# Kernel tuning notes

Measured on AMD Instinct MI355X. Metric: run time of the kernel, lower is better.

Reference implementation:

```python
import jax, jax.numpy as jnp
import numpy as np

MAX_DISTANCE = 10
SCALE = 0.01

def distance_bias(seq_len):
    # |i - j| clamped to MAX_DISTANCE, scaled
    idx = jnp.arange(seq_len, dtype=jnp.float32)
    d = jnp.abs(idx[None, :] - idx[:, None])
    return jnp.clip(d, 0.0, MAX_DISTANCE) * SCALE  # [S, S]

def setup_inputs() -> dict:
    key = jax.random.key(0)
    k1, k2 = jax.random.split(key)
    B, S, D_IN, D_OUT = 8, 2048, 1024, 1024
    x = jax.random.normal(k1, (B, S, D_IN), dtype=jnp.float32)
    W = jax.random.normal(k2, (D_IN, D_OUT), dtype=jnp.float32) * (1.0 / np.sqrt(D_IN))
    b = jnp.zeros((D_OUT,), dtype=jnp.float32)
    return {"x": x, "W": W, "b": b}

def reference(x, W, b):
    B, S, _ = x.shape
    f = x @ W + b                                   # [B, S, H]
    e = jnp.einsum('bsd,btd->bst', f, f)            # scores [B, S, S]
    e = e + distance_bias(S)[None, :, :]
    a = jax.nn.softmax(e, axis=-1)
    out = jnp.einsum('bst,btd->bsd', a, f)          # weighted sum [B, S, H]
    return out
```

## Files before the change

### kernel.cpp

```cpp
#include <hip/hip_runtime.h>
#include <hip/hip_bf16.h>
#include <stdint.h>

typedef __attribute__((ext_vector_type(8))) short bf16x8;
typedef __attribute__((ext_vector_type(4))) float f32x4;

static __device__ __forceinline__ unsigned short f2bf(float f) {
  union { float f; unsigned int u; } v; v.f = f;
  unsigned int u = v.u;
  u += 0x7FFFu + ((u >> 16) & 1u);
  return (unsigned short)(u >> 16);
}
static __device__ __forceinline__ float bf2f(unsigned short h) {
  union { unsigned int u; float f; } v; v.u = ((unsigned int)h) << 16; return v.f;
}

typedef __attribute__((address_space(1))) void gvoid;
typedef __attribute__((address_space(3))) void lvoid;
static __device__ __forceinline__ void gload_lds16(const void* gp, void* lp) {
  __builtin_amdgcn_global_load_lds((gvoid*)gp, (lvoid*)lp, 16, 0, 0);
}

__global__ __launch_bounds__(256) void k_convX(const float* __restrict__ X,
                                               unsigned short* __restrict__ Xb) {
  size_t i = ((size_t)blockIdx.x * 256 + threadIdx.x) * 8;
  const size_t stride = (size_t)4096 * 256 * 8;
  for (; i < (size_t)16777216; i += stride) {
    float4 v0 = *(const float4*)(X + i), v1 = *(const float4*)(X + i + 4);
    unsigned short h[8];
    h[0]=f2bf(v0.x); h[1]=f2bf(v0.y); h[2]=f2bf(v0.z); h[3]=f2bf(v0.w);
    h[4]=f2bf(v1.x); h[5]=f2bf(v1.y); h[6]=f2bf(v1.z); h[7]=f2bf(v1.w);
    *(uint4*)(Xb + i) = *(uint4*)h;
  }
}

__global__ __launch_bounds__(256) void k_convW(const float* __restrict__ W,
                                               unsigned short* __restrict__ Wt) {
  __shared__ __align__(16) unsigned short lds[64][72];
  const int tid = threadIdx.x;
  const int n0 = blockIdx.x * 64, k0 = blockIdx.y * 64;
  for (int i = 0; i < 4; ++i) {
    int c = i * 256 + tid;
    int r = c >> 4, c4 = (c & 15) * 4;
    float4 v = *(const float4*)(W + (size_t)(k0 + r) * 1024 + n0 + c4);
    unsigned short* p = &lds[r][c4];
    p[0] = f2bf(v.x); p[1] = f2bf(v.y); p[2] = f2bf(v.z); p[3] = f2bf(v.w);
  }
  __syncthreads();
  for (int i = 0; i < 2; ++i) {
    int c = i * 256 + tid;
    int n = c >> 3, k8 = (c & 7) * 8;
    unsigned short tmp[8];
    for (int j = 0; j < 8; ++j) tmp[j] = lds[k8 + j][n];
    *(uint4*)(Wt + (size_t)(n0 + n) * 1024 + k0 + k8) = *(uint4*)tmp;
  }
}

__global__ __launch_bounds__(256) void k_transF(const unsigned short* __restrict__ F,
                                                unsigned short* __restrict__ Ft) {
  __shared__ __align__(16) unsigned short lds[64][72];
  const int tid = threadIdx.x;
  const int t0 = blockIdx.x * 64, d0 = blockIdx.y * 64;
  const unsigned short* Fb = F + (size_t)blockIdx.z * 2048 * 1024;
  unsigned short* Ftb = Ft + (size_t)blockIdx.z * 1024 * 2048;
  for (int i = 0; i < 2; ++i) {
    int c = i * 256 + tid;
    int r = c >> 3, d8 = (c & 7) * 8;
    *(uint4*)(&lds[r][d8]) = *(const uint4*)(Fb + (size_t)(t0 + r) * 1024 + d0 + d8);
  }
  __syncthreads();
  for (int i = 0; i < 2; ++i) {
    int c = i * 256 + tid;
    int d = c >> 3, t8 = (c & 7) * 8;
    unsigned short tmp[8];
    for (int j = 0; j < 8; ++j) tmp[j] = lds[t8 + j][d];
    *(uint4*)(Ftb + (size_t)(d0 + d) * 2048 + t0 + t8) = *(uint4*)tmp;
  }
}


template<int NT>
__device__ __forceinline__ void gemm_core(
    const unsigned short* __restrict__ Ag, int lda, int ar0,
    const unsigned short* __restrict__ Bg, int ldb, int br0,
    unsigned short* __restrict__ As, unsigned short* __restrict__ Bs,
    f32x4 (&acc)[8][4]) {
  const int tid = threadIdx.x, lane = tid & 63, wid = tid >> 6;
  const int wr = wid >> 2, wc = wid & 3;
  const int rl = lane & 15;
  const int rslot = (((lane >> 4) ^ (lane & 3) ^ ((lane >> 2) & 3))) * 8;
  const int q = tid >> 2;
  const int sslot = (((tid & 3) ^ (q & 3) ^ ((q >> 2) & 3))) * 8;

#define STAGE_T(dstbase, src, ld, r0, kt)                                      \
  _Pragma("unroll")                                                            \
  for (int r_ = 0; r_ < 2; ++r_)                                               \
    gload_lds16((src) + (size_t)((r0) + r_ * 128 + q) * (ld) + (kt) * 32 + sslot, \
                (char*)(dstbase) + r_ * 8192 + wid * 1024);

  STAGE_T(As + 0 * 8192, Ag, lda, ar0, 0)
  STAGE_T(Bs + 0 * 8192, Bg, ldb, br0, 0)
  STAGE_T(As + 1 * 8192, Ag, lda, ar0, 1)
  STAGE_T(Bs + 1 * 8192, Bg, ldb, br0, 1)
  STAGE_T(As + 2 * 8192, Ag, lda, ar0, 2)
  STAGE_T(Bs + 2 * 8192, Bg, ldb, br0, 2)
  asm volatile("s_waitcnt vmcnt(8)" ::: "memory");
  __builtin_amdgcn_s_barrier();

  bf16x8 a[4], b[4], a2[4];
  for (int t = 0; t < NT; ++t) {
    const int sl = t & 3;
    const int ps = (t + 3 < NT) ? (t + 3) : (NT - 1);
    const int psl = (t + 3) & 3;
    const unsigned short* Ab = As + sl * 8192;
    const unsigned short* Bb = Bs + sl * 8192;
#pragma unroll
    for (int m = 0; m < 4; ++m)
      a[m] = *(const bf16x8*)(Ab + (wr * 128 + m * 16 + rl) * 32 + rslot);
#pragma unroll
    for (int n = 0; n < 4; ++n)
      b[n] = *(const bf16x8*)(Bb + (wc * 64 + n * 16 + rl) * 32 + rslot);
    STAGE_T(As + psl * 8192, Ag, lda, ar0, ps)
    __builtin_amdgcn_s_barrier();
    asm volatile("s_waitcnt lgkmcnt(0)" ::: "memory");
    __builtin_amdgcn_s_setprio(1);
#pragma unroll
    for (int m = 0; m < 4; ++m)
#pragma unroll
      for (int n = 0; n < 4; ++n)
        acc[m][n] = __builtin_amdgcn_mfma_f32_16x16x32_bf16(a[m], b[n], acc[m][n], 0, 0, 0);
    __builtin_amdgcn_s_setprio(0);
    __builtin_amdgcn_s_barrier();
#pragma unroll
    for (int m = 0; m < 4; ++m)
      a2[m] = *(const bf16x8*)(Ab + (wr * 128 + (m + 4) * 16 + rl) * 32 + rslot);
    STAGE_T(Bs + psl * 8192, Bg, ldb, br0, ps)
    __builtin_amdgcn_s_barrier();
    asm volatile("s_waitcnt lgkmcnt(0)" ::: "memory");
    __builtin_amdgcn_s_setprio(1);
#pragma unroll
    for (int m = 0; m < 4; ++m)
#pragma unroll
      for (int n = 0; n < 4; ++n)
        acc[m + 4][n] = __builtin_amdgcn_mfma_f32_16x16x32_bf16(a2[m], b[n], acc[m + 4][n], 0, 0, 0);
    __builtin_amdgcn_s_setprio(0);
    asm volatile("s_waitcnt vmcnt(8)" ::: "memory");
    __builtin_amdgcn_s_barrier();
  }
  asm volatile("s_waitcnt vmcnt(0)" ::: "memory");
#undef STAGE_T
}

__global__ __launch_bounds__(512, 2) void k_gemm1(const unsigned short* __restrict__ Xb,
                                                  const unsigned short* __restrict__ Wt,
                                                  const float* __restrict__ bias,
                                                  unsigned short* __restrict__ F) {
  __shared__ __align__(16) unsigned short As[4 * 8192];
  __shared__ __align__(16) unsigned short Bs[4 * 8192];
  const int bid = blockIdx.x;
  const int swz = (bid & 7) * 32 + (bid >> 3);
  const int m0 = (swz >> 2) * 256, n0 = (swz & 3) * 256;
  f32x4 acc[8][4] = {};
  gemm_core<32>(Xb, 1024, m0, Wt, 1024, n0, As, Bs, acc);
  const int tid = threadIdx.x, lane = tid & 63, wid = tid >> 6;
  const int wr = wid >> 2, wc = wid & 3;
  const int r4 = (lane >> 4) * 4, cl = lane & 15;
#pragma unroll
  for (int n = 0; n < 4; ++n) {
    int col = n0 + wc * 64 + n * 16 + cl;
    float bv = bias[col];
#pragma unroll
    for (int m = 0; m < 8; ++m) {
      int row = m0 + wr * 128 + m * 16 + r4;
#pragma unroll
      for (int j = 0; j < 4; ++j)
        F[(size_t)(row + j) * 1024 + col] = f2bf(acc[m][n][j] + bv);
    }
  }
}

__global__ __launch_bounds__(512, 2) void k_gemm2(const unsigned short* __restrict__ F,
                                                  unsigned short* __restrict__ E) {
  __shared__ __align__(16) unsigned short As[4 * 8192];
  __shared__ __align__(16) unsigned short Bs[4 * 8192];
  const int bid = blockIdx.x;
  const int swz = (bid & 7) * 64 + (bid >> 3);
  const int z = swz >> 6;
  const int m0 = ((swz >> 3) & 7) * 256, n0 = (swz & 7) * 256;
  const unsigned short* Fb = F + (size_t)z * 2048 * 1024;
  unsigned short* Eb = E + (size_t)z * 2048 * 2048;
  f32x4 acc[8][4] = {};
  gemm_core<32>(Fb, 1024, m0, Fb, 1024, n0, As, Bs, acc);
  const int tid = threadIdx.x, lane = tid & 63, wid = tid >> 6;
  const int wr = wid >> 2, wc = wid & 3;
  const int r4 = (lane >> 4) * 4, cl = lane & 15;
#pragma unroll
  for (int m = 0; m < 8; ++m) {
    int row = m0 + wr * 128 + m * 16 + r4;
#pragma unroll
    for (int n = 0; n < 4; ++n) {
      int col = n0 + wc * 64 + n * 16 + cl;
#pragma unroll
      for (int j = 0; j < 4; ++j) {
        int rr = row + j;
        int d = rr - col; d = d < 0 ? -d : d; d = d > 10 ? 10 : d;
        Eb[(size_t)rr * 2048 + col] = f2bf(acc[m][n][j] + (float)d * 0.01f);
      }
    }
  }
}

__global__ __launch_bounds__(256) void k_softmax(unsigned short* __restrict__ E) {
  unsigned short* row = E + (size_t)blockIdx.x * 2048;
  const int tid = threadIdx.x, lane = tid & 63, w = tid >> 6;
  uint4 v = *(const uint4*)(row + tid * 8);
  float f[8];
  const unsigned int* up = (const unsigned int*)&v;
  for (int i = 0; i < 4; ++i) {
    f[2*i]   = bf2f((unsigned short)(up[i] & 0xFFFF));
    f[2*i+1] = bf2f((unsigned short)(up[i] >> 16));
  }
  float mx = f[0];
  for (int i = 1; i < 8; ++i) mx = fmaxf(mx, f[i]);
  for (int s = 32; s > 0; s >>= 1) mx = fmaxf(mx, __shfl_xor(mx, s));
  __shared__ float redm[4], reds[4];
  if (lane == 0) redm[w] = mx;
  __syncthreads();
  mx = fmaxf(fmaxf(redm[0], redm[1]), fmaxf(redm[2], redm[3]));
  float p[8], sum = 0.f;
  for (int i = 0; i < 8; ++i) { p[i] = __expf(f[i] - mx); sum += p[i]; }
  for (int s = 32; s > 0; s >>= 1) sum += __shfl_xor(sum, s);
  if (lane == 0) reds[w] = sum;
  __syncthreads();
  sum = reds[0] + reds[1] + reds[2] + reds[3];
  float inv = 1.0f / sum;
  unsigned short h[8];
  for (int i = 0; i < 8; ++i) h[i] = f2bf(p[i] * inv);
  *(uint4*)(row + tid * 8) = *(uint4*)h;
}

__global__ __launch_bounds__(512, 2) void k_gemm3(const unsigned short* __restrict__ P,
                                                  const unsigned short* __restrict__ Ft,
                                                  float* __restrict__ out) {
  __shared__ __align__(16) unsigned short As[4 * 8192];
  __shared__ __align__(16) unsigned short Bs[4 * 8192];
  const int bid = blockIdx.x;
  const int swz = (bid & 7) * 32 + (bid >> 3);
  const int z = swz >> 5;
  const int m0 = ((swz >> 2) & 7) * 256, n0 = (swz & 3) * 256;
  const unsigned short* Pb = P + (size_t)z * 2048 * 2048;
  const unsigned short* Ftb = Ft + (size_t)z * 1024 * 2048;
  float* outb = out + (size_t)z * 2048 * 1024;
  f32x4 acc[8][4] = {};
  gemm_core<64>(Pb, 2048, m0, Ftb, 2048, n0, As, Bs, acc);
  const int tid = threadIdx.x, lane = tid & 63, wid = tid >> 6;
  const int wr = wid >> 2, wc = wid & 3;
  const int r4 = (lane >> 4) * 4, cl = lane & 15;
#pragma unroll
  for (int m = 0; m < 8; ++m) {
    int row = m0 + wr * 128 + m * 16 + r4;
#pragma unroll
    for (int n = 0; n < 4; ++n) {
      int col = n0 + wc * 64 + n * 16 + cl;
#pragma unroll
      for (int j = 0; j < 4; ++j)
        outb[(size_t)(row + j) * 1024 + col] = acc[m][n][j];
    }
  }
}

extern "C" void kernel_launch(void* const* d_in, const int* in_sizes, int n_in,
                              void* d_out, int out_size, void* d_ws, size_t ws_size,
                              hipStream_t stream) {
  const float* x = (const float*)d_in[0];
  const float* W = (const float*)d_in[1];
  const float* b = (const float*)d_in[2];
  float* out = (float*)d_out;

  unsigned short* Wt = (unsigned short*)d_ws;
  unsigned short* F  = (unsigned short*)((char*)d_ws + (2ull   << 20));
  unsigned short* Ft = (unsigned short*)((char*)d_ws + (34ull  << 20));
  unsigned short* E  = (unsigned short*)((char*)d_ws + (66ull  << 20));
  unsigned short* Xb = (unsigned short*)((char*)d_ws + (130ull << 20));

  k_convW  <<<dim3(16, 16),    256, 0, stream>>>(W, Wt);
  k_convX  <<<dim3(4096),      256, 0, stream>>>(x, Xb);
  k_gemm1  <<<dim3(256),       512, 0, stream>>>(Xb, Wt, b, F);
  k_transF <<<dim3(32, 16, 8), 256, 0, stream>>>(F, Ft);
  k_gemm2  <<<dim3(512),       512, 0, stream>>>(F, E);
  k_softmax<<<dim3(16384),     256, 0, stream>>>(E);
  k_gemm3  <<<dim3(256),       512, 0, stream>>>(E, Ft, out);
}
```

Before: 353.6 us.

## Exploit symmetry of F·Fᵀ in score GEMM and use wave-per-row softmax

The score GEMM now computes only the upper-triangular 256x256 tiles (36 per batch instead of 64) and writes the mirrored tile as a transpose staged through LDS. This is valid because F·Fᵀ is symmetric and the distance bias is symmetric too. The softmax kernel now processes one row per wavefront, with four rows per block, which removes the shared-memory reductions and __syncthreads. The cost is an extra LDS transpose pass with several barriers in the off-diagonal blocks, plus a small serial loop to map block index to tile.

```diff
diff --git a/kernel.cpp b/kernel.cpp
--- a/kernel.cpp
+++ b/kernel.cpp
@@ -184,9 +184,11 @@
   __shared__ __align__(16) unsigned short As[4 * 8192];
   __shared__ __align__(16) unsigned short Bs[4 * 8192];
   const int bid = blockIdx.x;
-  const int swz = (bid & 7) * 64 + (bid >> 3);
-  const int z = swz >> 6;
-  const int m0 = ((swz >> 3) & 7) * 256, n0 = (swz & 7) * 256;
+  const int z = bid & 7;
+  int rem = bid >> 3, bi = 0;
+  while (rem >= 8 - bi) { rem -= 8 - bi; ++bi; }
+  const int bj = bi + rem;
+  const int m0 = bi * 256, n0 = bj * 256;
   const unsigned short* Fb = F + (size_t)z * 2048 * 1024;
   unsigned short* Eb = E + (size_t)z * 2048 * 2048;
   f32x4 acc[8][4] = {};
@@ -208,35 +210,73 @@
       }
     }
   }
+  if (bi == bj) return;
+  __syncthreads();
+  unsigned short* lt = As;
+  for (int c = 0; c < 4; ++c) {
+    if (wr == (c >> 1)) {
+      const int mbase = (c & 1) * 4;
+#pragma unroll
+      for (int mm = 0; mm < 4; ++mm) {
+        const int m = mbase + mm;
+        const int row = m0 + wr * 128 + m * 16 + r4;
+#pragma unroll
+        for (int n = 0; n < 4; ++n) {
+          const int col = wc * 64 + n * 16 + cl;
+          const int colg = n0 + col;
+          unsigned short hh[4];
+#pragma unroll
+          for (int j = 0; j < 4; ++j) {
+            int rr = row + j;
+            int d = rr - colg; d = d < 0 ? -d : d; d = d > 10 ? 10 : d;
+            hh[j] = f2bf(acc[m][n][j] + (float)d * 0.01f);
+          }
+          *(uint2*)(lt + col * 72 + mm * 16 + r4) = *(uint2*)hh;
+        }
+      }
+    }
+    __syncthreads();
+    const int oc = tid >> 1, h = tid & 1;
+    unsigned short* dst = Eb + (size_t)(n0 + oc) * 2048 + m0 + c * 64 + h * 32;
+    const unsigned short* srcL = lt + oc * 72 + h * 32;
+#pragma unroll
+    for (int i = 0; i < 4; ++i)
+      *(uint4*)(dst + i * 8) = *(const uint4*)(srcL + i * 8);
+    __syncthreads();
+  }
 }
 
 __global__ __launch_bounds__(256) void k_softmax(unsigned short* __restrict__ E) {
-  unsigned short* row = E + (size_t)blockIdx.x * 2048;
   const int tid = threadIdx.x, lane = tid & 63, w = tid >> 6;
-  uint4 v = *(const uint4*)(row + tid * 8);
-  float f[8];
-  const unsigned int* up = (const unsigned int*)&v;
+  unsigned short* row = E + ((size_t)blockIdx.x * 4 + w) * 2048;
+  uint4 v[4];
+  float f[32];
+#pragma unroll
   for (int i = 0; i < 4; ++i) {
-    f[2*i]   = bf2f((unsigned short)(up[i] & 0xFFFF));
-    f[2*i+1] = bf2f((unsigned short)(up[i] >> 16));
+    v[i] = ((const uint4*)row)[i * 64 + lane];
+    const unsigned int* up = (const unsigned int*)&v[i];
+#pragma unroll
+    for (int k = 0; k < 4; ++k) {
+      f[i * 8 + 2 * k]     = bf2f((unsigned short)(up[k] & 0xFFFF));
+      f[i * 8 + 2 * k + 1] = bf2f((unsigned short)(up[k] >> 16));
+    }
   }
   float mx = f[0];
-  for (int i = 1; i < 8; ++i) mx = fmaxf(mx, f[i]);
+#pragma unroll
+  for (int i = 1; i < 32; ++i) mx = fmaxf(mx, f[i]);
   for (int s = 32; s > 0; s >>= 1) mx = fmaxf(mx, __shfl_xor(mx, s));
-  __shared__ float redm[4], reds[4];
-  if (lane == 0) redm[w] = mx;
-  __syncthreads();
-  mx = fmaxf(fmaxf(redm[0], redm[1]), fmaxf(redm[2], redm[3]));
-  float p[8], sum = 0.f;
-  for (int i = 0; i < 8; ++i) { p[i] = __expf(f[i] - mx); sum += p[i]; }
+  float sum = 0.f;
+#pragma unroll
+  for (int i = 0; i < 32; ++i) { f[i] = __expf(f[i] - mx); sum += f[i]; }
   for (int s = 32; s > 0; s >>= 1) sum += __shfl_xor(sum, s);
-  if (lane == 0) reds[w] = sum;
-  __syncthreads();
-  sum = reds[0] + reds[1] + reds[2] + reds[3];
-  float inv = 1.0f / sum;
-  unsigned short h[8];
-  for (int i = 0; i < 8; ++i) h[i] = f2bf(p[i] * inv);
-  *(uint4*)(row + tid * 8) = *(uint4*)h;
+  const float inv = 1.0f / sum;
+#pragma unroll
+  for (int i = 0; i < 4; ++i) {
+    unsigned short hh[8];
+#pragma unroll
+    for (int k = 0; k < 8; ++k) hh[k] = f2bf(f[i * 8 + k] * inv);
+    ((uint4*)row)[i * 64 + lane] = *(uint4*)hh;
+  }
 }
 
 __global__ __launch_bounds__(512, 2) void k_gemm3(const unsigned short* __restrict__ P,
@@ -287,7 +327,7 @@
   k_convX  <<<dim3(4096),      256, 0, stream>>>(x, Xb);
   k_gemm1  <<<dim3(256),       512, 0, stream>>>(Xb, Wt, b, F);
   k_transF <<<dim3(32, 16, 8), 256, 0, stream>>>(F, Ft);
-  k_gemm2  <<<dim3(512),       512, 0, stream>>>(F, E);
-  k_softmax<<<dim3(16384),     256, 0, stream>>>(E);
+  k_gemm2  <<<dim3(288),       512, 0, stream>>>(F, E);
+  k_softmax<<<dim3(4096),      256, 0, stream>>>(E);
   k_gemm3  <<<dim3(256),       512, 0, stream>>>(E, Ft, out);
 }
```

Result: slower. 436.6 us (+23.5%).
